# Performance work log

Hardware: AMD Instinct MI355X
Metric: run time of the kernel (lower is better)

## Reference

```python
import jax, jax.numpy as jnp
import numpy as np

B, S, D, H = 4, 2048, 1024, 16
HD = D // H


def setup_inputs() -> dict:
    key = jax.random.key(0)
    ks = jax.random.split(key, 12)
    scale = 1.0 / np.sqrt(D)
    q = jax.random.normal(ks[0], (B, S, D), jnp.float32)
    k = jax.random.normal(ks[1], (B, S, D), jnp.float32)
    v = jax.random.normal(ks[2], (B, S, D), jnp.float32)
    mask = jax.random.randint(ks[3], (B, S, S), 0, 2).astype(bool)
    Wq = jax.random.normal(ks[4], (D, D), jnp.float32) * scale
    bq = jnp.zeros((D,), jnp.float32)
    Wk = jax.random.normal(ks[5], (D, D), jnp.float32) * scale
    bk = jnp.zeros((D,), jnp.float32)
    Wv = jax.random.normal(ks[6], (D, D), jnp.float32) * scale
    bv = jnp.zeros((D,), jnp.float32)
    Wo = jax.random.normal(ks[7], (D, D), jnp.float32) * scale
    bo = jnp.zeros((D,), jnp.float32)
    return {"q": q, "k": k, "v": v, "mask": mask,
            "Wq": Wq, "bq": bq, "Wk": Wk, "bk": bk,
            "Wv": Wv, "bv": bv, "Wo": Wo, "bo": bo}


def reference(q, k, v, mask, Wq, bq, Wk, bk, Wv, bv, Wo, bo):
    # project and split heads: [B,S,D] -> [B,H,S,HD]
    def split_heads(x, W, b):
        y = x @ W + b
        return y.reshape(B, S, H, HD).transpose(0, 2, 1, 3)

    Q = split_heads(q, Wq, bq)
    K = split_heads(k, Wk, bk)
    V = split_heads(v, Wv, bv)
    inv_sqrt_dk = 1.0 / np.sqrt(HD)
    scores = jnp.einsum('bhqd,bhkd->bhqk', Q, K) * inv_sqrt_dk
    scores = jnp.where(mask[:, None, :, :], -1e9, scores)
    attn = jax.nn.softmax(scores, axis=-1)
    ctx = jnp.einsum('bhqk,bhkd->bhqd', attn, V)  # [B,H,S,HD]
    ctx = ctx.transpose(0, 2, 1, 3).reshape(B, S, D)
    return ctx @ Wo + bo
```

## Files before the change

kernel.cpp:

```cpp
#include <hip/hip_runtime.h>
#include <stdint.h>

#define B_ 4
#define S_ 2048
#define D_ 1024
#define H_ 16
#define HD_ 64

typedef __attribute__((ext_vector_type(8))) __bf16          bf16x8;
typedef __attribute__((ext_vector_type(8))) unsigned short  u16x8;
typedef __attribute__((ext_vector_type(4))) unsigned short  u16x4;
typedef __attribute__((ext_vector_type(4))) float           f32x4;
typedef __attribute__((ext_vector_type(16))) float          f32x16;
typedef unsigned short u16;
typedef unsigned int   u32;
typedef unsigned long long u64;

union BF8 { u16x8 u; bf16x8 b; u32 w[4]; };

__device__ __forceinline__ u16 f2bf(float f) {
  union { float f; uint32_t u; } v; v.f = f;
  uint32_t r = (v.u + 0x7FFFu + ((v.u >> 16) & 1u)) >> 16;
  return (u16)r;
}

__device__ __forceinline__ u32 cvtpk(float lo, float hi) {
  u32 r;
  asm("v_cvt_pk_bf16_f32 %0, %1, %2" : "=v"(r) : "v"(lo), "v"(hi));
  return r;
}

__device__ __forceinline__ float fexp2(float x) {
  float r;
  asm("v_exp_f32 %0, %1" : "=v"(r) : "v"(x));
  return r;
}

__device__ __forceinline__ float frcp(float x) {
  float r;
  asm("v_rcp_f32 %0, %1" : "=v"(r) : "v"(x));
  return r;
}

__device__ __forceinline__ void pswap(u32& a, u32& b) {
  asm("v_permlane32_swap_b32 %0, %1" : "+v"(a), "+v"(b));
}

__device__ __forceinline__ float andf(float x, u32 m) {
  union { float f; u32 u; } v; v.f = x; v.u &= m; return v.f;
}

typedef const unsigned int __attribute__((address_space(1)))* gas1_t;
typedef unsigned int __attribute__((address_space(3)))*       las3_t;

__device__ __forceinline__ void gll16(const void* g, void* l) {
  __builtin_amdgcn_global_load_lds((gas1_t)g, (las3_t)l, 16, 0, 0);
}

#define MFMA32(a, b, c) __builtin_amdgcn_mfma_f32_32x32x16_bf16((a), (b), (c), 0, 0, 0)

__global__ __launch_bounds__(256) void wt_k(const float* __restrict__ Wq, const float* __restrict__ Wk,
                                            const float* __restrict__ Wv, const float* __restrict__ Wo,
                                            u16* __restrict__ Tq, u16* __restrict__ Tk,
                                            u16* __restrict__ Tv, u16* __restrict__ To) {
  __shared__ float tile[64][65];
  int t = threadIdx.x;
  int wi = blockIdx.x;
  int z = wi >> 8, rem = wi & 255;
  int bx = rem & 15, by = rem >> 4;
  const float* src; u16* dst;
  switch (z) {
    case 0: src = Wq; dst = Tq; break;
    case 1: src = Wk; dst = Tk; break;
    case 2: src = Wv; dst = Tv; break;
    default: src = Wo; dst = To; break;
  }
  int k0 = bx * 64, n0 = by * 64;
#pragma unroll
  for (int it = 0; it < 4; ++it) {
    int idx = it * 256 + t;
    int r = idx >> 4, c = idx & 15;
    float4 v = *(const float4*)(src + (size_t)(k0 + r) * 1024 + n0 + c * 4);
    tile[r][c * 4 + 0] = v.x; tile[r][c * 4 + 1] = v.y;
    tile[r][c * 4 + 2] = v.z; tile[r][c * 4 + 3] = v.w;
  }
  __syncthreads();
#pragma unroll
  for (int it = 0; it < 2; ++it) {
    int idx = it * 256 + t;
    int n = idx >> 3, kc = idx & 7;
    u16x8 o;
#pragma unroll
    for (int j = 0; j < 8; ++j) o[j] = f2bf(tile[kc * 8 + j][n]);
    *(u16x8*)(dst + (size_t)(n0 + n) * 1024 + k0 + kc * 8) = o;
  }
}

__global__ __launch_bounds__(256) void maskpack_k(const void* __restrict__ mraw,
                                                  u64* __restrict__ mout) {
  const u32* hdr = (const u32*)mraw;
  int t = threadIdx.x;
  int lane = t & 63;
  u32 hv = hdr[lane];
  bool isf = (hv == 0x3F800000u);
  u64 bigm = __ballot(hv > 1u && !isf);
  u64 fm = __ballot(isf);
  int fmt = (__popcll(fm) > 8) ? 2 : ((bigm != 0ull) ? 0 : 1);
  size_t idx = (size_t)blockIdx.x * 256 + t;
  u64 bits = 0;
  if (fmt == 0) {
    const u64* p = (const u64*)((const uint8_t*)mraw + idx * 64);
#pragma unroll
    for (int j = 0; j < 8; ++j) {
      u64 v = p[j];
#pragma unroll
      for (int kk = 0; kk < 8; ++kk)
        bits |= (u64)(((v >> (8 * kk)) & 0xFFull) != 0) << (j * 8 + kk);
    }
  } else if (fmt == 1) {
    const int* p = ((const int*)mraw) + idx * 64;
#pragma unroll
    for (int j = 0; j < 64; ++j) bits |= (u64)(p[j] != 0) << j;
  } else {
    const u32* p = ((const u32*)mraw) + idx * 64;
#pragma unroll
    for (int j = 0; j < 64; ++j) bits |= (u64)((p[j] << 1) != 0) << j;
  }
  mout[idx] = bits;
}

__global__ __launch_bounds__(256) void proj3_k(const float* __restrict__ Aq, const float* __restrict__ Ak,
                                               const float* __restrict__ Av,
                                               const u16* __restrict__ Tq, const u16* __restrict__ Tk,
                                               const u16* __restrict__ Tv,
                                               const float* __restrict__ bq, const float* __restrict__ bk,
                                               const float* __restrict__ bv,
                                               u16* __restrict__ Qh, u16* __restrict__ Kh,
                                               u16* __restrict__ Vt, float qscale) {
  int g = blockIdx.x >> 9, bid = blockIdx.x & 511;
  const float* A; const u16* Bt; const float* bias; u16* outp; float scale;
  if (g == 0) { A = Aq; Bt = Tq; bias = bq; outp = Qh; scale = qscale; }
  else if (g == 1) { A = Ak; Bt = Tk; bias = bk; outp = Kh; scale = 1.0f; }
  else { A = Av; Bt = Tv; bias = bv; outp = Vt; scale = 1.0f; }
  int xcd = bid & 7, loc = bid >> 3;
  int mt = xcd * 8 + (loc & 7), nt = loc >> 3;
  int m0 = mt * 128, n0 = nt * 128;
  int t = threadIdx.x, w = t >> 6, lane = t & 63;
  int l15 = lane & 15, l4 = lane >> 4;
  int wm = w >> 1, wn = w & 1;
  __shared__ __align__(16) char smem[16384];
  const f32x4 vzero = {0.f, 0.f, 0.f, 0.f};
  f32x4 acc[4][4];
#pragma unroll
  for (int a = 0; a < 4; ++a)
#pragma unroll
    for (int c = 0; c < 4; ++c) acc[a][c] = vzero;

  int arow = t >> 1, ahalf = t & 1;
  const float* abase = A + (size_t)(m0 + arow) * 1024 + ahalf * 16;
  int aswz = (arow >> 1) & 3;
  char* adst0 = smem + arow * 64 + (((2 * ahalf) ^ aswz) << 4);
  char* adst1 = smem + arow * 64 + (((2 * ahalf + 1) ^ aswz) << 4);

  for (int k0 = 0; k0 < 1024; k0 += 32) {
    const float4* ap = (const float4*)(abase + k0);
    float4 a0 = ap[0], a1 = ap[1], a2 = ap[2], a3 = ap[3];
#pragma unroll
    for (int i = 0; i < 2; ++i) {
      int chunk = i * 256 + w * 64 + lane;
      int row = chunk >> 2, slot = chunk & 3;
      int sc = slot ^ ((row >> 1) & 3);
      gll16(Bt + (size_t)(n0 + row) * 1024 + k0 + sc * 8, smem + 8192 + (i * 256 + w * 64) * 16);
    }
    uint4 wv0, wv1;
    wv0.x = cvtpk(a0.x, a0.y); wv0.y = cvtpk(a0.z, a0.w);
    wv0.z = cvtpk(a1.x, a1.y); wv0.w = cvtpk(a1.z, a1.w);
    wv1.x = cvtpk(a2.x, a2.y); wv1.y = cvtpk(a2.z, a2.w);
    wv1.z = cvtpk(a3.x, a3.y); wv1.w = cvtpk(a3.z, a3.w);
    *(uint4*)adst0 = wv0;
    *(uint4*)adst1 = wv1;
    __syncthreads();
    BF8 am[4], bn[4];
#pragma unroll
    for (int mb = 0; mb < 4; ++mb) {
      int row = wm * 64 + mb * 16 + l15;
      int sl = l4 ^ ((row >> 1) & 3);
      am[mb].u = *(const u16x8*)(smem + row * 64 + sl * 16);
    }
#pragma unroll
    for (int nb = 0; nb < 4; ++nb) {
      int row = wn * 64 + nb * 16 + l15;
      int sl = l4 ^ ((row >> 1) & 3);
      bn[nb].u = *(const u16x8*)(smem + 8192 + row * 64 + sl * 16);
    }
#pragma unroll
    for (int mb = 0; mb < 4; ++mb)
#pragma unroll
      for (int nb = 0; nb < 4; ++nb)
        acc[mb][nb] = __builtin_amdgcn_mfma_f32_16x16x32_bf16(am[mb].b, bn[nb].b, acc[mb][nb], 0, 0, 0);
    __syncthreads();
  }
  if (g == 2) {
#pragma unroll
    for (int mb = 0; mb < 4; ++mb)
#pragma unroll
      for (int nb = 0; nb < 4; ++nb) {
        int no = n0 + wn * 64 + nb * 16 + l15;
        int h = no >> 6, hd = no & 63;
        int m = m0 + wm * 64 + mb * 16 + l4 * 4;
        int bb = m >> 11, s = m & 2047;
        float bsv = bias[no];
        u16x4 ov;
#pragma unroll
        for (int r = 0; r < 4; ++r) ov[r] = f2bf(acc[mb][nb][r] + bsv);
        *(u16x4*)(outp + (((size_t)bb * H_ + h) * HD_ + hd) * S_ + s) = ov;
      }
  } else {
#pragma unroll
    for (int mb = 0; mb < 4; ++mb)
#pragma unroll
      for (int nb = 0; nb < 4; ++nb)
#pragma unroll
        for (int r = 0; r < 4; ++r) {
          int grow = m0 + wm * 64 + mb * 16 + l4 * 4 + r;
          int gcol = n0 + wn * 64 + nb * 16 + l15;
          float v = (acc[mb][nb][r] + bias[gcol]) * scale;
          int bb = grow >> 11, s = grow & 2047, h = gcol >> 6, hd = gcol & 63;
          outp[(((size_t)bb * H_ + h) * S_ + s) * HD_ + hd] = f2bf(v);
        }
  }
}

__global__ __launch_bounds__(256) void gemmo_k(const u16* __restrict__ A,
                                               const u16* __restrict__ Bt,
                                               const float* __restrict__ bias,
                                               float* __restrict__ outp) {
  int bid = blockIdx.x;
  int xcd = bid & 7, loc = bid >> 3;
  int mt = xcd * 8 + (loc & 7), nt = loc >> 3;
  int m0 = mt * 128, n0 = nt * 128;
  int t = threadIdx.x, w = t >> 6, lane = t & 63;
  int l15 = lane & 15, l4 = lane >> 4;
  int wm = w >> 1, wn = w & 1;
  __shared__ __align__(16) char smem[16384];
  const f32x4 vzero = {0.f, 0.f, 0.f, 0.f};
  f32x4 acc[4][4];
#pragma unroll
  for (int a = 0; a < 4; ++a)
#pragma unroll
    for (int c = 0; c < 4; ++c) acc[a][c] = vzero;

  for (int k0 = 0; k0 < 1024; k0 += 32) {
#pragma unroll
    for (int i = 0; i < 2; ++i) {
      int chunk = i * 256 + w * 64 + lane;
      int row = chunk >> 2, slot = chunk & 3;
      int sc = slot ^ ((row >> 1) & 3);
      gll16(A + (size_t)(m0 + row) * 1024 + k0 + sc * 8, smem + (i * 256 + w * 64) * 16);
      gll16(Bt + (size_t)(n0 + row) * 1024 + k0 + sc * 8, smem + 8192 + (i * 256 + w * 64) * 16);
    }
    __syncthreads();
    BF8 am[4], bn[4];
#pragma unroll
    for (int mb = 0; mb < 4; ++mb) {
      int row = wm * 64 + mb * 16 + l15;
      int sl = l4 ^ ((row >> 1) & 3);
      am[mb].u = *(const u16x8*)(smem + row * 64 + sl * 16);
    }
#pragma unroll
    for (int nb = 0; nb < 4; ++nb) {
      int row = wn * 64 + nb * 16 + l15;
      int sl = l4 ^ ((row >> 1) & 3);
      bn[nb].u = *(const u16x8*)(smem + 8192 + row * 64 + sl * 16);
    }
#pragma unroll
    for (int mb = 0; mb < 4; ++mb)
#pragma unroll
      for (int nb = 0; nb < 4; ++nb)
        acc[mb][nb] = __builtin_amdgcn_mfma_f32_16x16x32_bf16(am[mb].b, bn[nb].b, acc[mb][nb], 0, 0, 0);
    __syncthreads();
  }
#pragma unroll
  for (int mb = 0; mb < 4; ++mb)
#pragma unroll
    for (int nb = 0; nb < 4; ++nb)
#pragma unroll
      for (int r = 0; r < 4; ++r) {
        int grow = m0 + wm * 64 + mb * 16 + l4 * 4 + r;
        int gcol = n0 + wn * 64 + nb * 16 + l15;
        outp[(size_t)grow * 1024 + gcol] = acc[mb][nb][r] + bias[gcol];
      }
}

__global__ __launch_bounds__(256) void flash_k(const u16* __restrict__ Qh,
                                               const u16* __restrict__ Kh,
                                               const u16* __restrict__ Vt,
                                               const u64* __restrict__ mb,
                                               u16* __restrict__ ctx) {
  int bid = blockIdx.x;
  int xcd = bid & 7, loc = bid >> 3;
  int bh = xcd * 8 + (loc & 7);
  int qblk = loc >> 3;
  int b = bh >> 4, h = bh & 15;
  int t = threadIdx.x, w = t >> 6, lane = t & 63;
  int l31 = lane & 31, l5 = lane >> 5;
  __shared__ __align__(16) char smem[32768];

  int q0 = qblk * 128 + w * 32;
  const u16* kbase = Kh + (size_t)bh * S_ * HD_;
  const u16* vbase = Vt + (size_t)bh * HD_ * S_;
  const uint2* mrow = ((const uint2*)mb) + ((size_t)b * S_ + q0 + l31) * 32;

  const u16* qbase = Qh + ((size_t)bh * S_ + q0 + l31) * HD_;
  BF8 qf[4];
#pragma unroll
  for (int dk = 0; dk < 4; ++dk) qf[dk].u = *(const u16x8*)(qbase + dk * 16 + l5 * 8);

  int koff0[4], koffB[4];
#pragma unroll
  for (int dk = 0; dk < 4; ++dk) {
    int s0_ = (dk * 2 + l5) ^ (l31 & 7) ^ (l31 >> 3);
    koff0[dk] = l31 * 128 + s0_ * 16;
    koffB[dk] = 4096 + l31 * 128 + ((s0_ ^ 4) * 16);
  }

  BF8 onesf;
#pragma unroll
  for (int i = 0; i < 8; ++i) onesf.u[i] = 0x3F80;

  f32x16 o0, o1, lac, zv;
#pragma unroll
  for (int r = 0; r < 16; ++r) { o0[r] = 0.f; o1[r] = 0.f; lac[r] = 0.f; zv[r] = 0.f; }

#define STAGE(KT, BUF)                                                          \
  do {                                                                          \
    char* Kd = smem + (BUF);                                                    \
    int k0s = (KT) * 64;                                                        \
    _Pragma("unroll") for (int i_ = 0; i_ < 2; ++i_) {                          \
      int c_ = i_ * 256 + t;                                                    \
      int row_ = c_ >> 3, sl_ = c_ & 7;                                         \
      int sc_ = sl_ ^ (row_ & 7) ^ (row_ >> 3);                                 \
      int cw_ = (i_ * 256 + w * 64) * 16;                                       \
      gll16(kbase + (size_t)(k0s + row_) * HD_ + sc_ * 8, Kd + cw_);            \
      gll16(vbase + (size_t)row_ * S_ + k0s + sc_ * 8, Kd + 8192 + cw_);        \
    }                                                                           \
  } while (0)

#define MKFRAG(FR, A0, B0, C0, D0)                                              \
  do {                                                                          \
    u32 xx0 = (A0), xx1 = (C0), yy0 = (B0), yy1 = (D0);                         \
    pswap(xx0, xx1); pswap(yy0, yy1);                                           \
    FR.w[0] = xx0; FR.w[1] = yy0; FR.w[2] = xx1; FR.w[3] = yy1;                 \
  } while (0)

#define PVS(FR, KC)                                                             \
  do {                                                                          \
    lac = MFMA32(FR.b, onesf.b, lac);                                           \
    BF8 vf0, vf1;                                                               \
    vf0.u = *(const u16x8*)(Kb + 8192 + koff0[(KC)]);                           \
    vf1.u = *(const u16x8*)(Kb + 8192 + koffB[(KC)]);                           \
    o0 = MFMA32(FR.b, vf0.b, o0);                                               \
    o1 = MFMA32(FR.b, vf1.b, o1);                                               \
  } while (0)

#define FTILE(KT, BUF, OBUF, ISLAST)                                            \
  {                                                                             \
    __syncthreads();                                                            \
    uint2 mw = mrow[(KT)];                                                      \
    if (!(ISLAST)) STAGE((KT) + 1, OBUF);                                       \
    const char* Kb = smem + (BUF);                                              \
    f32x16 sa0, sa1;                                                            \
    __builtin_amdgcn_s_setprio(1);                                              \
    {                                                                           \
      BF8 kf0, kf1;                                                             \
      kf0.u = *(const u16x8*)(Kb + koff0[0]);                                   \
      kf1.u = *(const u16x8*)(Kb + koffB[0]);                                   \
      sa0 = MFMA32(kf0.b, qf[0].b, zv);                                         \
      sa1 = MFMA32(kf1.b, qf[0].b, zv);                                         \
    }                                                                           \
    _Pragma("unroll") for (int dk = 1; dk < 4; ++dk) {                          \
      BF8 kf0, kf1;                                                             \
      kf0.u = *(const u16x8*)(Kb + koff0[dk]);                                  \
      kf1.u = *(const u16x8*)(Kb + koffB[dk]);                                  \
      sa0 = MFMA32(kf0.b, qf[dk].b, sa0);                                       \
      sa1 = MFMA32(kf1.b, qf[dk].b, sa1);                                       \
    }                                                                           \
    __builtin_amdgcn_s_setprio(0);                                              \
    u32 nw0 = ~(mw.x >> (l5 * 4));                                              \
    u32 nw1 = ~(mw.y >> (l5 * 4));                                              \
    _Pragma("unroll") for (int r = 0; r < 16; ++r) {                            \
      const int pp = (r & 3) + 8 * (r >> 2);                                    \
      sa0[r] = andf(fexp2(sa0[r]), (u32)__builtin_amdgcn_sbfe((int)nw0, pp, 1));\
      sa1[r] = andf(fexp2(sa1[r]), (u32)__builtin_amdgcn_sbfe((int)nw1, pp, 1));\
    }                                                                           \
    u32 pk0[8], pk1[8];                                                         \
    _Pragma("unroll") for (int i = 0; i < 8; ++i) {                             \
      pk0[i] = cvtpk(sa0[2 * i], sa0[2 * i + 1]);                               \
      pk1[i] = cvtpk(sa1[2 * i], sa1[2 * i + 1]);                               \
    }                                                                           \
    BF8 fr0, fr1, fr2, fr3;                                                     \
    MKFRAG(fr0, pk0[0], pk0[1], pk0[2], pk0[3]);                                \
    MKFRAG(fr1, pk0[4], pk0[5], pk0[6], pk0[7]);                                \
    MKFRAG(fr2, pk1[0], pk1[1], pk1[2], pk1[3]);                                \
    MKFRAG(fr3, pk1[4], pk1[5], pk1[6], pk1[7]);                                \
    __builtin_amdgcn_s_setprio(1);                                              \
    PVS(fr0, 0); PVS(fr1, 1); PVS(fr2, 2); PVS(fr3, 3);                         \
    __builtin_amdgcn_s_setprio(0);                                              \
  }

  STAGE(0, 0);
  for (int kt2 = 0; kt2 < 16; ++kt2) {
    FTILE(2 * kt2, 0, 16384, false);
    FTILE(2 * kt2 + 1, 16384, 0, (kt2 == 15));
  }

#pragma unroll
  for (int r = 0; r < 16; ++r) {
    float inv = frcp(lac[r] + 1e-35f);
    int q = (r & 3) + 8 * (r >> 2) + 4 * l5;
    size_t base = ((size_t)b * S_ + q0 + q) * D_ + h * HD_;
    ctx[base + l31]      = f2bf(o0[r] * inv);
    ctx[base + 32 + l31] = f2bf(o1[r] * inv);
  }
#undef STAGE
#undef MKFRAG
#undef PVS
#undef FTILE
}

extern "C" void kernel_launch(void* const* d_in, const int* in_sizes, int n_in,
                              void* d_out, int out_size, void* d_ws, size_t ws_size,
                              hipStream_t stream) {
  (void)in_sizes; (void)n_in; (void)out_size; (void)ws_size;
  const float* q  = (const float*)d_in[0];
  const float* k  = (const float*)d_in[1];
  const float* v  = (const float*)d_in[2];
  const void*  mk = d_in[3];
  const float* Wq = (const float*)d_in[4];
  const float* bq = (const float*)d_in[5];
  const float* Wk = (const float*)d_in[6];
  const float* bk = (const float*)d_in[7];
  const float* Wv = (const float*)d_in[8];
  const float* bv = (const float*)d_in[9];
  const float* Wo = (const float*)d_in[10];
  const float* bo = (const float*)d_in[11];

  char* ws = (char*)d_ws;
  u16* ctx  = (u16*)(ws + 16777216);
  u64* mc   = (u64*)(ws + 33554432);
  u16* Tq   = (u16*)(ws + 50331648);
  u16* Tk   = (u16*)(ws + 52428800);
  u16* Tv   = (u16*)(ws + 54525952);
  u16* To   = (u16*)(ws + 56623104);
  u16* Qh   = (u16*)(ws + 58720256);
  u16* Kh   = (u16*)(ws + 75497472);
  u16* Vt   = (u16*)(ws + 92274688);

  const float QSCALE = 0.18033688011112042f;

  maskpack_k<<<1024, 256, 0, stream>>>(mk, mc);
  wt_k<<<1024, 256, 0, stream>>>(Wq, Wk, Wv, Wo, Tq, Tk, Tv, To);
  proj3_k<<<1536, 256, 0, stream>>>(q, k, v, Tq, Tk, Tv,
                                    bq, bk, bv, Qh, Kh, Vt, QSCALE);
  flash_k<<<1024, 256, 0, stream>>>(Qh, Kh, Vt, mc, ctx);
  gemmo_k<<<512, 256, 0, stream>>>(ctx, To, bo, (float*)d_out);
}
```

Measured before the change: 282.0 us.

## Double-buffer LDS in QKV projection GEMM to overlap loads with MFMA

The QKV projection GEMM now uses two LDS buffers for both the A and B tiles. The next k-tile's A registers and B global-to-LDS loads are issued right after the barrier, so they overlap the MFMA work on the current tile, and one __syncthreads per iteration is dropped. This doubles LDS use to 32KB per block, which may lower occupancy. Correctness now depends on the single barrier protecting buffer reuse across two iterations, including the asynchronous gll16 writes.

After: 264.1 us. -6.4%, faster.

```diff
diff --git a/kernel.cpp b/kernel.cpp
--- a/kernel.cpp
+++ b/kernel.cpp
@@ -148,7 +148,7 @@
   int t = threadIdx.x, w = t >> 6, lane = t & 63;
   int l15 = lane & 15, l4 = lane >> 4;
   int wm = w >> 1, wn = w & 1;
-  __shared__ __align__(16) char smem[16384];
+  __shared__ __align__(16) char smem[32768];
   const f32x4 vzero = {0.f, 0.f, 0.f, 0.f};
   f32x4 acc[4][4];
 #pragma unroll
@@ -159,46 +159,67 @@
   int arow = t >> 1, ahalf = t & 1;
   const float* abase = A + (size_t)(m0 + arow) * 1024 + ahalf * 16;
   int aswz = (arow >> 1) & 3;
-  char* adst0 = smem + arow * 64 + (((2 * ahalf) ^ aswz) << 4);
-  char* adst1 = smem + arow * 64 + (((2 * ahalf + 1) ^ aswz) << 4);
-
-  for (int k0 = 0; k0 < 1024; k0 += 32) {
-    const float4* ap = (const float4*)(abase + k0);
-    float4 a0 = ap[0], a1 = ap[1], a2 = ap[2], a3 = ap[3];
-#pragma unroll
-    for (int i = 0; i < 2; ++i) {
-      int chunk = i * 256 + w * 64 + lane;
-      int row = chunk >> 2, slot = chunk & 3;
-      int sc = slot ^ ((row >> 1) & 3);
-      gll16(Bt + (size_t)(n0 + row) * 1024 + k0 + sc * 8, smem + 8192 + (i * 256 + w * 64) * 16);
-    }
+  int aoff0 = arow * 64 + (((2 * ahalf) ^ aswz) << 4);
+  int aoff1 = arow * 64 + (((2 * ahalf + 1) ^ aswz) << 4);
+
+  int brow[2], bsc[2], bdst[2];
+#pragma unroll
+  for (int i = 0; i < 2; ++i) {
+    int chunk = i * 256 + w * 64 + lane;
+    brow[i] = chunk >> 2;
+    int slot = chunk & 3;
+    bsc[i] = slot ^ ((brow[i] >> 1) & 3);
+    bdst[i] = (i * 256 + w * 64) * 16;
+  }
+
+  float4 a0, a1, a2, a3;
+  {
+    const float4* ap = (const float4*)abase;
+    a0 = ap[0]; a1 = ap[1]; a2 = ap[2]; a3 = ap[3];
+  }
+#pragma unroll
+  for (int i = 0; i < 2; ++i)
+    gll16(Bt + (size_t)(n0 + brow[i]) * 1024 + bsc[i] * 8, smem + 16384 + bdst[i]);
+
+  for (int kt = 0; kt < 32; ++kt) {
+    int buf = kt & 1;
+    char* bA = smem + buf * 8192;
     uint4 wv0, wv1;
     wv0.x = cvtpk(a0.x, a0.y); wv0.y = cvtpk(a0.z, a0.w);
     wv0.z = cvtpk(a1.x, a1.y); wv0.w = cvtpk(a1.z, a1.w);
     wv1.x = cvtpk(a2.x, a2.y); wv1.y = cvtpk(a2.z, a2.w);
     wv1.z = cvtpk(a3.x, a3.y); wv1.w = cvtpk(a3.z, a3.w);
-    *(uint4*)adst0 = wv0;
-    *(uint4*)adst1 = wv1;
+    *(uint4*)(bA + aoff0) = wv0;
+    *(uint4*)(bA + aoff1) = wv1;
     __syncthreads();
+    if (kt < 31) {
+      int k0n = (kt + 1) * 32;
+      const float4* ap = (const float4*)(abase + k0n);
+      a0 = ap[0]; a1 = ap[1]; a2 = ap[2]; a3 = ap[3];
+      char* bB = smem + 16384 + (buf ^ 1) * 8192;
+#pragma unroll
+      for (int i = 0; i < 2; ++i)
+        gll16(Bt + (size_t)(n0 + brow[i]) * 1024 + k0n + bsc[i] * 8, bB + bdst[i]);
+    }
+    const char* bBr = smem + 16384 + buf * 8192;
     BF8 am[4], bn[4];
 #pragma unroll
     for (int mb = 0; mb < 4; ++mb) {
       int row = wm * 64 + mb * 16 + l15;
       int sl = l4 ^ ((row >> 1) & 3);
-      am[mb].u = *(const u16x8*)(smem + row * 64 + sl * 16);
+      am[mb].u = *(const u16x8*)(bA + row * 64 + sl * 16);
     }
 #pragma unroll
     for (int nb = 0; nb < 4; ++nb) {
       int row = wn * 64 + nb * 16 + l15;
       int sl = l4 ^ ((row >> 1) & 3);
-      bn[nb].u = *(const u16x8*)(smem + 8192 + row * 64 + sl * 16);
+      bn[nb].u = *(const u16x8*)(bBr + row * 64 + sl * 16);
     }
 #pragma unroll
     for (int mb = 0; mb < 4; ++mb)
 #pragma unroll
       for (int nb = 0; nb < 4; ++nb)
         acc[mb][nb] = __builtin_amdgcn_mfma_f32_16x16x32_bf16(am[mb].b, bn[nb].b, acc[mb][nb], 0, 0, 0);
-    __syncthreads();
   }
   if (g == 2) {
 #pragma unroll
```
